# Kernel tuning notes

Measured on AMD Instinct MI355X. Metric: run time of the kernel, lower is better.

## Reference

```python
import jax, jax.numpy as jnp
import numpy as np

N_FEATURES = 256
RAND_RANGE = 100.0


def _random_embed(x):
    """Deterministic pseudo-random embedding: each scalar in x seeds a counter-based
    RNG producing N_FEATURES uniforms in [0, RAND_RANGE). (JAX threefry replaces
    Python's Mersenne Twister; same structure: value-seeded deterministic uniforms.)"""
    flat = jax.lax.stop_gradient(x).reshape(-1)
    seeds = jax.lax.bitcast_convert_type(flat, jnp.uint32)  # value -> integer seed
    base = jax.random.key(42)
    keys = jax.vmap(lambda s: jax.random.fold_in(base, s))(seeds)
    emb = jax.vmap(lambda k: jax.random.uniform(k, (N_FEATURES,), minval=0.0, maxval=RAND_RANGE))(keys)
    return emb.reshape(x.shape + (N_FEATURES,))  # [B, S, F]


def setup_inputs() -> dict:
    key = jax.random.key(0)
    kx, kw, kb = jax.random.split(key, 3)
    x = jax.random.normal(kx, (256, 512), dtype=jnp.float32)
    W = jax.random.normal(kw, (N_FEATURES, N_FEATURES), dtype=jnp.float32) * 0.05
    b = jax.random.normal(kb, (N_FEATURES,), dtype=jnp.float32) * 0.05
    return {"x": x, "W": W, "b": b}


def reference(x, W, b):
    emb = _random_embed(x)                      # [B, S, F]
    out = jnp.einsum('bsf,gf->bsg', emb, W) + b  # nn.Linear: emb @ W.T + b
    return out
```

## Files before the change

kernel.cpp:

```cpp
#include <hip/hip_runtime.h>
#include <stdint.h>

#define F 256
#define R 64
#define THREADS 256
#define GCH 32
#define NCH (F / GCH)
#define CH_SLOTS (GCH * F / 8)

typedef __attribute__((ext_vector_type(8))) short short8;
typedef __attribute__((ext_vector_type(4))) float floatx4;

__device__ __forceinline__ uint32_t rotl32(uint32_t x, int d) {
  return __builtin_amdgcn_alignbit(x, x, (uint32_t)(32 - d));
}

struct TFK { uint32_t k0, k1, k2, a1, a2, a3, a4, a5; };

__device__ __forceinline__ TFK mkkeys(uint32_t k0, uint32_t k1) {
  TFK K;
  K.k0 = k0; K.k1 = k1; K.k2 = k0 ^ k1 ^ 0x1BD11BDAu;
  K.a1 = K.k2 + 1u; K.a2 = k0 + 2u; K.a3 = k1 + 3u;
  K.a4 = K.k2 + 4u; K.a5 = k0 + 5u;
  return K;
}

__device__ __forceinline__ void tf_one(const TFK& K, uint32_t& x0, uint32_t& x1) {
  x0 += K.k0; x1 += K.k1;
#define TF1(r) x0 += x1; x1 = rotl32(x1, r); x1 ^= x0;
  TF1(13) TF1(15) TF1(26) TF1(6)   x0 += K.k1; x1 += K.a1;
  TF1(17) TF1(29) TF1(16) TF1(24)  x0 += K.k2; x1 += K.a2;
  TF1(13) TF1(15) TF1(26) TF1(6)   x0 += K.k0; x1 += K.a3;
  TF1(17) TF1(29) TF1(16) TF1(24)  x0 += K.k1; x1 += K.a4;
  TF1(13) TF1(15) TF1(26) TF1(6)   x0 += K.k2; x1 += K.a5;
#undef TF1
}

__device__ __forceinline__ void tf_pair(const TFK& K, uint32_t i,
                                        uint32_t& oa, uint32_t& ob) {
  uint32_t a0 = K.k0, a1 = K.k1 + i;
  uint32_t b0 = K.k0, b1 = K.k1 + i + 1u;
#define TF2(r)  a0 += a1; b0 += b1;                         \
                a1 = rotl32(a1, r); b1 = rotl32(b1, r);     \
                a1 ^= a0; b1 ^= b0;
#define INJ2(u, v) a0 += (u); b0 += (u); a1 += (v); b1 += (v);
  TF2(13) TF2(15) TF2(26) TF2(6)   INJ2(K.k1, K.a1)
  TF2(17) TF2(29) TF2(16) TF2(24)  INJ2(K.k2, K.a2)
  TF2(13) TF2(15) TF2(26) TF2(6)   INJ2(K.k0, K.a3)
  TF2(17) TF2(29) TF2(16) TF2(24)  INJ2(K.k1, K.a4)
  TF2(13) TF2(15) TF2(26) TF2(6)   INJ2(K.k2, K.a5)
#undef TF2
#undef INJ2
  oa = a0 ^ a1;
  ob = b0 ^ b1;
}

__device__ __forceinline__ uint32_t featpack(const TFK& K, uint32_t i) {
  uint32_t xa, xb;
  tf_pair(K, i, xa, xb);
  uint32_t ulo = __float_as_uint((float)xa * 2.3283064365386963e-8f);
  uint32_t uhi = __float_as_uint((float)xb * 2.3283064365386963e-8f);
  ulo += 0x7FFFu + ((ulo >> 16) & 1u);
  uhi += 0x7FFFu + ((uhi >> 16) & 1u);
  return __builtin_amdgcn_perm(uhi, ulo, 0x07060302u);
}

__device__ __forceinline__ uint32_t f2bf(float f) {
  uint32_t u = __float_as_uint(f);
  u += 0x7FFFu + ((u >> 16) & 1u);
  return u >> 16;
}

__global__ __launch_bounds__(256) void femb_conv(const float* __restrict__ W,
                                                 uint16_t* __restrict__ ws) {
  int s = blockIdx.x * 256 + threadIdx.x;
  int gt = s >> 10;
  int c = (s >> 5) & 31;
  int g = s & 31;
  const float4* src = (const float4*)(W + (size_t)(gt * GCH + g) * F + c * 8);
  float4 v0 = src[0], v1 = src[1];
  short8 o;
  o[0] = (short)f2bf(v0.x); o[1] = (short)f2bf(v0.y);
  o[2] = (short)f2bf(v0.z); o[3] = (short)f2bf(v0.w);
  o[4] = (short)f2bf(v1.x); o[5] = (short)f2bf(v1.y);
  o[6] = (short)f2bf(v1.z); o[7] = (short)f2bf(v1.w);
  *(short8*)(ws + (size_t)s * 8) = o;
}

__global__ __launch_bounds__(THREADS, 4) void femb_main(
    const float* __restrict__ x, const uint16_t* __restrict__ Wbf,
    const float* __restrict__ bias, float* __restrict__ out) {
  const int tid  = threadIdx.x;
  const int lane = tid & 63;
  const int wave = tid >> 6;
  const int qd   = lane >> 4;
  const int l16  = lane & 15;
  const size_t row0 = (size_t)blockIdx.x * R;
  const int myrow = (int)row0 + wave * 16 + l16;

  float xv = x[myrow];

  TFK K42 = mkkeys(0u, 42u);
  uint32_t s0 = 0u, s1 = __float_as_uint(xv);
  tf_one(K42, s0, s1);
  const TFK K = mkkeys(s0, s1);

  short8 afrag[8];
  #pragma unroll
  for (int kt = 0; kt < 8; ++kt) {
    const uint32_t fb = (uint32_t)(kt * 32 + qd * 8);
    uint32_t w32[4];
    #pragma unroll
    for (int p = 0; p < 4; ++p)
      w32[p] = featpack(K, fb + 2 * p);
    union { uint32_t w[4]; short8 s; } u;
    u.w[0] = w32[0]; u.w[1] = w32[1]; u.w[2] = w32[2]; u.w[3] = w32[3];
    afrag[kt] = u.s;
  }

  #pragma unroll 1
  for (int gt = 0; gt < NCH; ++gt) {
    const uint16_t* Wc = Wbf + (size_t)gt * CH_SLOTS * 8;
    floatx4 acc[2];
    acc[0] = (floatx4){0.f, 0.f, 0.f, 0.f};
    acc[1] = (floatx4){0.f, 0.f, 0.f, 0.f};
    #pragma unroll
    for (int kt = 0; kt < 8; ++kt) {
      int c = kt * 4 + qd;
      #pragma unroll
      for (int n = 0; n < 2; ++n) {
        short8 b = *(const short8*)(Wc + (size_t)(c * 32 + n * 16 + l16) * 8);
        acc[n] = __builtin_amdgcn_mfma_f32_16x16x32_bf16(afrag[kt], b, acc[n], 0, 0, 0);
      }
    }

    #pragma unroll
    for (int n = 0; n < 2; ++n) {
      int g = gt * GCH + n * 16 + l16;
      float bg = bias[g];
      #pragma unroll
      for (int reg = 0; reg < 4; ++reg) {
        size_t grow = row0 + (size_t)wave * 16 + qd * 4 + reg;
        out[grow * F + g] = acc[n][reg] + bg;
      }
    }
  }
}

extern "C" void kernel_launch(void* const* d_in, const int* in_sizes, int n_in,
                              void* d_out, int out_size, void* d_ws, size_t ws_size,
                              hipStream_t stream) {
  const float* x = (const float*)d_in[0];
  const float* W = (const float*)d_in[1];
  const float* b = (const float*)d_in[2];
  float* out = (float*)d_out;
  uint16_t* wsbf = (uint16_t*)d_ws;
  const int nrows = in_sizes[0];
  const int blocks = nrows / R;

  hipLaunchKernelGGL(femb_conv, dim3((F * F / 8) / 256), dim3(256), 0, stream, W, wsbf);
  hipLaunchKernelGGL(femb_main, dim3(blocks), dim3(THREADS), 0, stream,
                     x, wsbf, b, out);
}
```

Before: 195.1 us.

## Software-pipeline threefry feature generation with LDS-staged MFMA over multiple row tiles

Each block now handles four 64-row tiles instead of one. While the MFMA work for the current tile runs, the threefry features for the next tile are generated in the same loop. W chunks are double-buffered in LDS through global_load_lds DMA instead of being read directly from global memory per wave. The aim is to overlap the ALU-heavy RNG with matrix work and stores, and to share W loads across waves. In exchange the grid has a quarter as many blocks, launch bounds drop to 2 blocks per CU, register pressure rises from holding two fragment sets, and each block pays for an extra prologue pass over all W chunks.

```diff
diff --git a/kernel.cpp b/kernel.cpp
--- a/kernel.cpp
+++ b/kernel.cpp
@@ -7,6 +7,7 @@
 #define GCH 32
 #define NCH (F / GCH)
 #define CH_SLOTS (GCH * F / 8)
+#define TPB 4
 
 typedef __attribute__((ext_vector_type(8))) short short8;
 typedef __attribute__((ext_vector_type(4))) float floatx4;
@@ -65,10 +66,34 @@
   return __builtin_amdgcn_perm(uhi, ulo, 0x07060302u);
 }
 
+__device__ __forceinline__ short8 quad(const TFK& K, uint32_t fb) {
+  uint32_t w32[4];
+  #pragma unroll
+  for (int p = 0; p < 4; ++p) w32[p] = featpack(K, fb + 2u * p);
+  union { uint32_t w[4]; short8 s; } u;
+  u.w[0] = w32[0]; u.w[1] = w32[1]; u.w[2] = w32[2]; u.w[3] = w32[3];
+  return u.s;
+}
+
 __device__ __forceinline__ uint32_t f2bf(float f) {
   uint32_t u = __float_as_uint(f);
   u += 0x7FFFu + ((u >> 16) & 1u);
   return u >> 16;
+}
+
+__device__ __forceinline__ void gl_lds16(const void* gptr, void* lptr) {
+  __builtin_amdgcn_global_load_lds(
+      (const __attribute__((address_space(1))) uint32_t*)gptr,
+      (__attribute__((address_space(3))) uint32_t*)lptr, 16, 0, 0);
+}
+
+__device__ __forceinline__ void dma_chunk(const uint16_t* __restrict__ src,
+                                          uint16_t* dst, int wave, int lane) {
+  #pragma unroll
+  for (int it = 0; it < CH_SLOTS / THREADS; ++it) {
+    int sbase = it * THREADS + wave * 64;
+    gl_lds16(src + (size_t)(sbase + lane) * 8, dst + (size_t)sbase * 8);
+  }
 }
 
 __global__ __launch_bounds__(256) void femb_conv(const float* __restrict__ W,
@@ -87,62 +112,82 @@
   *(short8*)(ws + (size_t)s * 8) = o;
 }
 
-__global__ __launch_bounds__(THREADS, 4) void femb_main(
+__global__ __launch_bounds__(THREADS, 2) void femb_main(
     const float* __restrict__ x, const uint16_t* __restrict__ Wbf,
     const float* __restrict__ bias, float* __restrict__ out) {
+  __shared__ uint16_t sW[2][GCH * F];
+
   const int tid  = threadIdx.x;
   const int lane = tid & 63;
   const int wave = tid >> 6;
   const int qd   = lane >> 4;
   const int l16  = lane & 15;
-  const size_t row0 = (size_t)blockIdx.x * R;
-  const int myrow = (int)row0 + wave * 16 + l16;
-
-  float xv = x[myrow];
-
-  TFK K42 = mkkeys(0u, 42u);
-  uint32_t s0 = 0u, s1 = __float_as_uint(xv);
-  tf_one(K42, s0, s1);
-  const TFK K = mkkeys(s0, s1);
-
-  short8 afrag[8];
-  #pragma unroll
-  for (int kt = 0; kt < 8; ++kt) {
-    const uint32_t fb = (uint32_t)(kt * 32 + qd * 8);
-    uint32_t w32[4];
+  const int tb0  = blockIdx.x * TPB;
+  const int rl   = wave * 16 + l16;
+
+  const TFK K42 = mkkeys(0u, 42u);
+
+  float xn = x[(size_t)tb0 * R + rl];
+
+  short8 afragC[8];
+  #pragma unroll 1
+  for (int t = -1; t < TPB; ++t) {
+    const bool hasNext  = (t + 1 < TPB);
+    const bool doCompute = (t >= 0);
+
+    TFK K2 = K42;
+    if (hasNext) {
+      uint32_t u0 = 0u, u1 = __float_as_uint(xn);
+      tf_one(K42, u0, u1);
+      K2 = mkkeys(u0, u1);
+    }
+    if (t + 2 < TPB) xn = x[(size_t)(tb0 + t + 2) * R + rl];
+
+    const size_t growbase = doCompute
+        ? ((size_t)(tb0 + t) * R + (size_t)(wave * 16 + qd * 4))
+        : 0;
+
+    short8 afragN[8];
     #pragma unroll
-    for (int p = 0; p < 4; ++p)
-      w32[p] = featpack(K, fb + 2 * p);
-    union { uint32_t w[4]; short8 s; } u;
-    u.w[0] = w32[0]; u.w[1] = w32[1]; u.w[2] = w32[2]; u.w[3] = w32[3];
-    afrag[kt] = u.s;
-  }
-
-  #pragma unroll 1
-  for (int gt = 0; gt < NCH; ++gt) {
-    const uint16_t* Wc = Wbf + (size_t)gt * CH_SLOTS * 8;
-    floatx4 acc[2];
-    acc[0] = (floatx4){0.f, 0.f, 0.f, 0.f};
-    acc[1] = (floatx4){0.f, 0.f, 0.f, 0.f};
-    #pragma unroll
-    for (int kt = 0; kt < 8; ++kt) {
-      int c = kt * 4 + qd;
-      #pragma unroll
-      for (int n = 0; n < 2; ++n) {
-        short8 b = *(const short8*)(Wc + (size_t)(c * 32 + n * 16 + l16) * 8);
-        acc[n] = __builtin_amdgcn_mfma_f32_16x16x32_bf16(afrag[kt], b, acc[n], 0, 0, 0);
+    for (int gt = 0; gt < NCH; ++gt) {
+      __syncthreads();
+
+      if (!((t == TPB - 1) && (gt == NCH - 1)))
+        dma_chunk(Wbf + (size_t)((gt + 1) & 7) * CH_SLOTS * 8,
+                  sW[(gt + 1) & 1], wave, lane);
+
+      if (hasNext)
+        afragN[gt] = quad(K2, (uint32_t)(gt * 32 + qd * 8));
+
+      if (doCompute) {
+        const uint16_t* buf = sW[gt & 1];
+        floatx4 acc[2];
+        acc[0] = (floatx4){0.f, 0.f, 0.f, 0.f};
+        acc[1] = (floatx4){0.f, 0.f, 0.f, 0.f};
+        #pragma unroll
+        for (int kt = 0; kt < 8; ++kt) {
+          int c = kt * 4 + qd;
+          #pragma unroll
+          for (int n = 0; n < 2; ++n) {
+            short8 b = *(const short8*)&buf[(size_t)(c * 32 + n * 16 + l16) * 8];
+            acc[n] = __builtin_amdgcn_mfma_f32_16x16x32_bf16(afragC[kt], b,
+                                                             acc[n], 0, 0, 0);
+          }
+        }
+        #pragma unroll
+        for (int n = 0; n < 2; ++n) {
+          int g = gt * GCH + n * 16 + l16;
+          float bg = bias[g];
+          #pragma unroll
+          for (int reg = 0; reg < 4; ++reg)
+            out[(growbase + reg) * F + g] = acc[n][reg] + bg;
+        }
       }
     }
 
-    #pragma unroll
-    for (int n = 0; n < 2; ++n) {
-      int g = gt * GCH + n * 16 + l16;
-      float bg = bias[g];
+    if (hasNext) {
       #pragma unroll
-      for (int reg = 0; reg < 4; ++reg) {
-        size_t grow = row0 + (size_t)wave * 16 + qd * 4 + reg;
-        out[grow * F + g] = acc[n][reg] + bg;
-      }
+      for (int i = 0; i < 8; ++i) afragC[i] = afragN[i];
     }
   }
 }
@@ -156,7 +201,7 @@
   float* out = (float*)d_out;
   uint16_t* wsbf = (uint16_t*)d_ws;
   const int nrows = in_sizes[0];
-  const int blocks = nrows / R;
+  const int blocks = nrows / (R * TPB);
 
   hipLaunchKernelGGL(femb_conv, dim3((F * F / 8) / 256), dim3(256), 0, stream, W, wsbf);
   hipLaunchKernelGGL(femb_main, dim3(blocks), dim3(THREADS), 0, stream,
```

Result: slower. 203.3 us (+4.3%).

## Interleave threefry feature generation with MFMA over K chunks, accumulate all outputs

Applied to the files above, without the earlier changes.

The loop order changes from output-column chunks to K chunks, with all 16 output tiles accumulated in registers. The A fragment for the next K chunk is generated with threefry while the current chunk's MFMAs and W loads are in flight, so ALU hashing overlaps matrix-core and memory work. The full afrag array is no longer held. This raises accumulator register use (64 floats), so launch bounds drop from 4 to 3 waves per unit, which may reduce occupancy.

```diff
diff --git a/kernel.cpp b/kernel.cpp
--- a/kernel.cpp
+++ b/kernel.cpp
@@ -65,6 +65,15 @@
   return __builtin_amdgcn_perm(uhi, ulo, 0x07060302u);
 }
 
+__device__ __forceinline__ short8 quad(const TFK& K, uint32_t fb) {
+  uint32_t w32[4];
+  #pragma unroll
+  for (int p = 0; p < 4; ++p) w32[p] = featpack(K, fb + 2u * p);
+  union { uint32_t w[4]; short8 s; } u;
+  u.w[0] = w32[0]; u.w[1] = w32[1]; u.w[2] = w32[2]; u.w[3] = w32[3];
+  return u.s;
+}
+
 __device__ __forceinline__ uint32_t f2bf(float f) {
   uint32_t u = __float_as_uint(f);
   u += 0x7FFFu + ((u >> 16) & 1u);
@@ -87,7 +96,7 @@
   *(short8*)(ws + (size_t)s * 8) = o;
 }
 
-__global__ __launch_bounds__(THREADS, 4) void femb_main(
+__global__ __launch_bounds__(THREADS, 3) void femb_main(
     const float* __restrict__ x, const uint16_t* __restrict__ Wbf,
     const float* __restrict__ bias, float* __restrict__ out) {
   const int tid  = threadIdx.x;
@@ -100,50 +109,60 @@
 
   float xv = x[myrow];
 
-  TFK K42 = mkkeys(0u, 42u);
-  uint32_t s0 = 0u, s1 = __float_as_uint(xv);
-  tf_one(K42, s0, s1);
-  const TFK K = mkkeys(s0, s1);
+  const TFK K42 = mkkeys(0u, 42u);
+  uint32_t u0 = 0u, u1 = __float_as_uint(xv);
+  tf_one(K42, u0, u1);
+  const TFK K = mkkeys(u0, u1);
 
-  short8 afrag[8];
+  short8 afragC = quad(K, (uint32_t)(qd * 8));
+
+  const uint16_t* wlane = Wbf + (size_t)(qd * 256 + l16 * 8);
+
+  floatx4 acc[16];
   #pragma unroll
-  for (int kt = 0; kt < 8; ++kt) {
-    const uint32_t fb = (uint32_t)(kt * 32 + qd * 8);
-    uint32_t w32[4];
+  for (int n = 0; n < 16; ++n) acc[n] = (floatx4){0.f, 0.f, 0.f, 0.f};
+
+  #pragma unroll 1
+  for (int kt = 0; kt < NCH; ++kt) {
+    const uint16_t* wk = wlane + (size_t)kt * 1024;
+    const uint32_t fb = (uint32_t)((kt + 1) * GCH + qd * 8);
+    const bool more = (kt + 1 < NCH);
+    uint32_t w0 = 0, w1 = 0, w2 = 0, w3 = 0;
+    short8 b[8];
+
     #pragma unroll
-    for (int p = 0; p < 4; ++p)
-      w32[p] = featpack(K, fb + 2 * p);
-    union { uint32_t w[4]; short8 s; } u;
-    u.w[0] = w32[0]; u.w[1] = w32[1]; u.w[2] = w32[2]; u.w[3] = w32[3];
-    afrag[kt] = u.s;
+    for (int n = 0; n < 8; ++n)
+      b[n] = *(const short8*)(wk + (n >> 1) * 8192 + (n & 1) * 128);
+    if (more) { w0 = featpack(K, fb); w1 = featpack(K, fb + 2u); }
+    #pragma unroll
+    for (int n = 0; n < 8; ++n)
+      acc[n] = __builtin_amdgcn_mfma_f32_16x16x32_bf16(afragC, b[n], acc[n],
+                                                       0, 0, 0);
+
+    #pragma unroll
+    for (int n = 0; n < 8; ++n)
+      b[n] = *(const short8*)(wk + ((n + 8) >> 1) * 8192 + (n & 1) * 128);
+    if (more) { w2 = featpack(K, fb + 4u); w3 = featpack(K, fb + 6u); }
+    #pragma unroll
+    for (int n = 0; n < 8; ++n)
+      acc[n + 8] = __builtin_amdgcn_mfma_f32_16x16x32_bf16(afragC, b[n],
+                                                           acc[n + 8], 0, 0, 0);
+
+    if (more) {
+      union { uint32_t w[4]; short8 s; } u;
+      u.w[0] = w0; u.w[1] = w1; u.w[2] = w2; u.w[3] = w3;
+      afragC = u.s;
+    }
   }
 
-  #pragma unroll 1
-  for (int gt = 0; gt < NCH; ++gt) {
-    const uint16_t* Wc = Wbf + (size_t)gt * CH_SLOTS * 8;
-    floatx4 acc[2];
-    acc[0] = (floatx4){0.f, 0.f, 0.f, 0.f};
-    acc[1] = (floatx4){0.f, 0.f, 0.f, 0.f};
+  const size_t growbase = row0 + (size_t)(wave * 16 + qd * 4);
+  #pragma unroll
+  for (int n = 0; n < 16; ++n) {
+    int g = n * 16 + l16;
+    float bg = bias[g];
     #pragma unroll
-    for (int kt = 0; kt < 8; ++kt) {
-      int c = kt * 4 + qd;
-      #pragma unroll
-      for (int n = 0; n < 2; ++n) {
-        short8 b = *(const short8*)(Wc + (size_t)(c * 32 + n * 16 + l16) * 8);
-        acc[n] = __builtin_amdgcn_mfma_f32_16x16x32_bf16(afrag[kt], b, acc[n], 0, 0, 0);
-      }
-    }
-
-    #pragma unroll
-    for (int n = 0; n < 2; ++n) {
-      int g = gt * GCH + n * 16 + l16;
-      float bg = bias[g];
-      #pragma unroll
-      for (int reg = 0; reg < 4; ++reg) {
-        size_t grow = row0 + (size_t)wave * 16 + qd * 4 + reg;
-        out[grow * F + g] = acc[n][reg] + bg;
-      }
-    }
+    for (int reg = 0; reg < 4; ++reg)
+      out[(growbase + reg) * F + g] = acc[n][reg] + bg;
   }
 }
 
```

New measurement: 214.3 us. +9.9%, slower.
